# Kernel tuning notes

Measured on AMD Instinct MI355X. Metric: run time of the kernel, lower is better.

## Reference

```python
import jax, jax.numpy as jnp
import numpy as np

DIM = 1536; NH = 12; HD = DIM // NH; C = HD // 2  # C = 64
F, H, W = 12, 16, 16; S = F * H * W  # 3072 tokens
NFPB = 3       # num_frame_per_block (block-causal granularity)
LOCAL = 6      # local_attn_size in frames
SINK = 1       # sink_size in frames
EPS = 1e-06


def setup_inputs():
    key = jax.random.key(0)
    ks = jax.random.split(key, 6)
    sc = 1.0 / np.sqrt(DIM)
    x = jax.random.normal(ks[0], (1, S, DIM), jnp.float32)
    Wq = jax.random.normal(ks[1], (DIM, DIM), jnp.float32) * sc
    Wk = jax.random.normal(ks[2], (DIM, DIM), jnp.float32) * sc
    Wv = jax.random.normal(ks[3], (DIM, DIM), jnp.float32) * sc
    Wo = jax.random.normal(ks[4], (DIM, DIM), jnp.float32) * sc
    zeros = jnp.zeros((DIM,), jnp.float32); ones = jnp.ones((DIM,), jnp.float32)
    # RoPE table: unit-modulus complex freqs stored as cos/sin, shape [1024, C]
    ang = jax.random.uniform(ks[5], (1024, C), jnp.float32) * (2.0 * np.pi)
    return dict(x=x, Wq=Wq, bq=zeros, Wk=Wk, bk=zeros, Wv=Wv, bv=zeros,
                Wo=Wo, bo=zeros, gq=ones, gk=ones,
                freqs_cos=jnp.cos(ang), freqs_sin=jnp.sin(ang), f=F, h=H, w=W)


def _rms_norm(x, g):
    y = x * jax.lax.rsqrt(jnp.mean(x * x, axis=-1, keepdims=True) + EPS)
    return y * g


def _pos_table(tab, f, h, w):
    # split [1024, C] into frame/height/width parts and broadcast to [f*h*w, C]
    cf = C - 2 * (C // 3); ch = C // 3
    tf = jnp.broadcast_to(tab[:f, :cf][:, None, None, :], (f, h, w, cf))
    th = jnp.broadcast_to(tab[:h, cf:cf + ch][None, :, None, :], (f, h, w, ch))
    tw = jnp.broadcast_to(tab[:w, cf + ch:][None, None, :, :], (f, h, w, ch))
    return jnp.concatenate([tf, th, tw], axis=-1).reshape(f * h * w, C)


def _rope(x, cosp, sinp):
    # complex multiply on consecutive (real, imag) pairs along head_dim
    b, s, n, d = x.shape
    xp = x.reshape(b, s, n, d // 2, 2)
    xr, xi = xp[..., 0], xp[..., 1]
    cp = cosp[None, :, None, :]; sp = sinp[None, :, None, :]
    out = jnp.stack([xr * cp - xi * sp, xr * sp + xi * cp], axis=-1)
    return out.reshape(b, s, n, d)


def reference(x, Wq, bq, Wk, bk, Wv, bv, Wo, bo, gq, gk, freqs_cos, freqs_sin, f, h, w):
    b, s, _ = x.shape
    q = _rms_norm(x @ Wq.T + bq, gq).reshape(b, s, NH, HD)
    k = _rms_norm(x @ Wk.T + bk, gk).reshape(b, s, NH, HD)
    v = (x @ Wv.T + bv).reshape(b, s, NH, HD)
    cosp = _pos_table(freqs_cos, f, h, w)
    sinp = _pos_table(freqs_sin, f, h, w)
    rq = _rope(q, cosp, sinp)
    rk = _rope(k, cosp, sinp)
    # block mask: block-causal (bidirectional inside a frame-block) + local window + sink
    idx = jnp.arange(s)
    frame = idx // (h * w)
    blk = frame // NFPB
    qb, kb = blk[:, None], blk[None, :]
    mask = (kb <= qb) & ((((qb - kb) * NFPB) < LOCAL) | (frame[None, :] < SINK))
    scores = jnp.einsum('bqnd,bknd->bnqk', rq, rk) * (HD ** -0.5)
    scores = jnp.where(mask[None, None], scores, jnp.finfo(scores.dtype).min)
    probs = jax.nn.softmax(scores, axis=-1)
    out = jnp.einsum('bnqk,bknd->bqnd', probs, v).reshape(b, s, DIM)
    return out @ Wo.T + bo
```

## Files before the change

kernel.cpp:

```cpp
#include <hip/hip_runtime.h>
#include <stdint.h>

typedef unsigned short u16;
typedef __attribute__((ext_vector_type(8))) short bf16x8;
typedef __attribute__((ext_vector_type(4))) short bf16x4;
typedef __attribute__((ext_vector_type(4))) float f32x4;

constexpr int DMODEL = 1536;
constexpr int SEQ    = 3072;
constexpr int NHEAD  = 12;
constexpr int HDIM   = 128;

__device__ __forceinline__ u16 f2bf(float f){
  union { float f; unsigned u; } v; v.f = f;
  return (u16)((v.u + 0x7fffu + ((v.u >> 16) & 1u)) >> 16);
}

__global__ __launch_bounds__(256) void cvt4_kernel(const float* __restrict__ src,
                                                   u16* __restrict__ dst, int n4){
  int i = blockIdx.x * 256 + threadIdx.x;
  if (i < n4){
    float4 f = ((const float4*)src)[i];
    ushort4 o;
    o.x = f2bf(f.x); o.y = f2bf(f.y); o.z = f2bf(f.z); o.w = f2bf(f.w);
    ((ushort4*)dst)[i] = o;
  }
}

__device__ __forceinline__ void gload16(const u16* g, u16* l){
  __builtin_amdgcn_global_load_lds((const __attribute__((address_space(1))) void*)g,
                                   (__attribute__((address_space(3))) void*)l, 16, 0, 0);
}

__device__ __forceinline__ void gemm_core(const u16* __restrict__ A, const u16* __restrict__ W,
    const float* __restrict__ bias, float* __restrict__ C, int m0, int n0,
    u16* As, u16* Bs)
{
  const int tid  = threadIdx.x;
  const int lane = tid & 63;
  const int wv   = tid >> 6;
  const int wm   = wv & 1, wn = wv >> 1;
  const int l15  = lane & 15, lg = lane >> 4;

  f32x4 acc[4][4];
#pragma unroll
  for (int i = 0; i < 4; i++)
#pragma unroll
    for (int j = 0; j < 4; j++){ f32x4 z = {0.f,0.f,0.f,0.f}; acc[i][j] = z; }

  const int r0 = wv * 16 + (lane >> 2);
  const int r1 = (wv + 4) * 16 + (lane >> 2);
  const int cc = (lane & 3) * 8;
  const u16* Ab = A + (size_t)m0 * DMODEL;
  const u16* Wb = W + (size_t)n0 * DMODEL;

  for (int k0 = 0; k0 < DMODEL; k0 += 32){
    gload16(Ab + (size_t)r0 * DMODEL + k0 + cc, As + wv * 512);
    gload16(Ab + (size_t)r1 * DMODEL + k0 + cc, As + (wv + 4) * 512);
    gload16(Wb + (size_t)r0 * DMODEL + k0 + cc, Bs + wv * 512);
    gload16(Wb + (size_t)r1 * DMODEL + k0 + cc, Bs + (wv + 4) * 512);
    __syncthreads();

    bf16x8 af[4], bfr[4];
#pragma unroll
    for (int mi = 0; mi < 4; mi++)
      af[mi]  = *(const bf16x8*)(As + (wm * 64 + mi * 16 + l15) * 32 + lg * 8);
#pragma unroll
    for (int ni = 0; ni < 4; ni++)
      bfr[ni] = *(const bf16x8*)(Bs + (wn * 64 + ni * 16 + l15) * 32 + lg * 8);
#pragma unroll
    for (int mi = 0; mi < 4; mi++)
#pragma unroll
      for (int ni = 0; ni < 4; ni++)
        acc[mi][ni] = __builtin_amdgcn_mfma_f32_16x16x32_bf16(af[mi], bfr[ni], acc[mi][ni], 0, 0, 0);
    __syncthreads();
  }

#pragma unroll
  for (int mi = 0; mi < 4; mi++){
    int row = m0 + wm * 64 + mi * 16 + (lg << 2);
#pragma unroll
    for (int ni = 0; ni < 4; ni++){
      int col = n0 + wn * 64 + ni * 16 + l15;
      float bvv = bias[col];
#pragma unroll
      for (int r = 0; r < 4; r++)
        C[(size_t)(row + r) * DMODEL + col] = acc[mi][ni][r] + bvv;
    }
  }
}

__global__ __launch_bounds__(256) void gemm_qkv(const u16* __restrict__ xb,
    const u16* __restrict__ wqb, const u16* __restrict__ wkb, const u16* __restrict__ wvb,
    const float* __restrict__ bq, const float* __restrict__ bk, const float* __restrict__ bv,
    float* __restrict__ qf, float* __restrict__ kf, float* __restrict__ vf)
{
  __shared__ u16 As[128 * 32], Bs[128 * 32];
  int mt = blockIdx.x, nt = blockIdx.y;
  int sel = nt / 12, ntl = nt % 12;
  const u16* W = sel == 0 ? wqb : (sel == 1 ? wkb : wvb);
  const float* bias = sel == 0 ? bq : (sel == 1 ? bk : bv);
  float* C = sel == 0 ? qf : (sel == 1 ? kf : vf);
  gemm_core(xb, W, bias, C, mt * 128, ntl * 128, As, Bs);
}

__global__ __launch_bounds__(256) void gemm_o(const u16* __restrict__ ab,
    const u16* __restrict__ wob, const float* __restrict__ bo, float* __restrict__ out)
{
  __shared__ u16 As[128 * 32], Bs[128 * 32];
  gemm_core(ab, wob, bo, out, blockIdx.x * 128, blockIdx.y * 128, As, Bs);
}

__global__ __launch_bounds__(256) void rmsrope_kernel(
    const float* __restrict__ qin, const float* __restrict__ kin,
    const float* __restrict__ gq, const float* __restrict__ gk,
    const float* __restrict__ fcos, const float* __restrict__ fsin,
    u16* __restrict__ rq, u16* __restrict__ rk)
{
  int s = blockIdx.x, t = threadIdx.x;
  int fi = s >> 8, hi2 = (s >> 4) & 15, wi = s & 15;
  __shared__ float red[4];

  for (int pass = 0; pass < 2; pass++){
    const float* in = pass ? kin : qin;
    const float* g  = pass ? gk  : gq;
    u16* outp       = pass ? rk  : rq;
    const float* row = in + (size_t)s * DMODEL;

    float v[6];
    float2 a = *(const float2*)(row + t * 6);
    float2 b = *(const float2*)(row + t * 6 + 2);
    float2 c = *(const float2*)(row + t * 6 + 4);
    v[0] = a.x; v[1] = a.y; v[2] = b.x; v[3] = b.y; v[4] = c.x; v[5] = c.y;

    float ss = 0.f;
#pragma unroll
    for (int j = 0; j < 6; j++) ss += v[j] * v[j];
#pragma unroll
    for (int m = 1; m < 64; m <<= 1) ss += __shfl_xor(ss, m);
    if ((t & 63) == 0) red[t >> 6] = ss;
    __syncthreads();
    float tot = red[0] + red[1] + red[2] + red[3];
    float scale = rsqrtf(tot * (1.0f / (float)DMODEL) + 1e-6f);

#pragma unroll
    for (int p = 0; p < 3; p++){
      int i  = t * 3 + p;
      int pi = i & 63;
      int idx = pi < 22 ? fi : (pi < 43 ? hi2 : wi);
      float cv = fcos[idx * 64 + pi];
      float sv = fsin[idx * 64 + pi];
      int d = t * 6 + 2 * p;
      float xr = v[2 * p]     * scale * g[d];
      float xi = v[2 * p + 1] * scale * g[d + 1];
      outp[(size_t)s * DMODEL + d]     = f2bf(xr * cv - xi * sv);
      outp[(size_t)s * DMODEL + d + 1] = f2bf(xr * sv + xi * cv);
    }
    __syncthreads();
  }
}

__global__ __launch_bounds__(256) void transpose_v(const float* __restrict__ vf, u16* __restrict__ vt)
{
  __shared__ float tile[32][33];
  int tx = threadIdx.x & 31, ty = threadIdx.x >> 5;
  int d0 = blockIdx.x * 32;
  int s0 = blockIdx.y * 32;
#pragma unroll
  for (int j = 0; j < 4; j++)
    tile[ty + j * 8][tx] = vf[(size_t)(s0 + ty + j * 8) * DMODEL + d0 + tx];
  __syncthreads();
  int px = ((tx & 15) >> 2) * 8 + ((tx >> 4) & 1) * 4 + (tx & 3);
#pragma unroll
  for (int j = 0; j < 4; j++)
    vt[(size_t)(d0 + ty + j * 8) * SEQ + s0 + px] = f2bf(tile[tx][ty + j * 8]);
}

__global__ __launch_bounds__(256, 2) void attn_kernel(const u16* __restrict__ rq,
    const u16* __restrict__ rk, const u16* __restrict__ vt, u16* __restrict__ ao)
{
  __shared__ u16 Ks[2][8192];
  __shared__ u16 Vs[2][8192];

  const int tid  = threadIdx.x;
  const int lane = tid & 63;
  const int wv   = tid >> 6;
  const int head = blockIdx.y;
  const int grp  = blockIdx.x / 12;
  const int rem  = blockIdx.x - grp * 12;
  const int qb   = 3 - grp;
  const int q_i  = qb * 12 + rem;
  const int q0   = q_i * 64 + wv * 16;
  const int l15  = lane & 15, lg = lane >> 4;
  const int swz  = (l15 & 7) << 4;
  const float sc = 0.08838834764831845f;

  int r0s = 0, r0e = 0, r1s = 0, r1e = 0;
  if      (qb == 0){ r0e = 768; }
  else if (qb == 1){ r0e = 1536; }
  else if (qb == 2){ r0e = 256; r1s = 768;  r1e = 2304; }
  else             { r0e = 256; r1s = 1536; r1e = 3072; }
  const int nt0 = (r0e - r0s) >> 6;
  const int nt  = nt0 + ((r1e - r1s) >> 6);

  const char* rkB = (const char*)rk;
  const char* vtB = (const char*)vt;

  auto k0_of = [&](int t){ return t < nt0 ? (r0s + t * 64) : (r1s + (t - nt0) * 64); };

  auto stage = [&](int buf, int k0){
    char* Kd = (char*)Ks[buf];
    char* Vd = (char*)Vs[buf];
#pragma unroll
    for (int c = 0; c < 4; c++){
      int o = c * 4096 + wv * 1024 + lane * 16;
      int row = o >> 8, colb = o & 255;
      gload16((const u16*)(rkB + (size_t)(k0 + row) * (DMODEL * 2) + head * (HDIM * 2)
                               + (colb ^ ((row & 7) << 4))),
              (u16*)(Kd + c * 4096 + wv * 1024));
    }
#pragma unroll
    for (int c = 0; c < 4; c++){
      int o = c * 4096 + wv * 1024 + lane * 16;
      int row = o >> 7, colb = o & 127;
      gload16((const u16*)(vtB + (size_t)(head * HDIM + row) * (SEQ * 2) + (size_t)k0 * 2
                               + (colb ^ ((row & 7) << 4))),
              (u16*)(Vd + c * 4096 + wv * 1024));
    }
  };

  bf16x8 qfr[4];
  const u16* qbase = rq + (size_t)(q0 + l15) * DMODEL + head * HDIM + lg * 8;
#pragma unroll
  for (int c = 0; c < 4; c++) qfr[c] = *(const bf16x8*)(qbase + c * 32);

  f32x4 oacc[8];
#pragma unroll
  for (int i = 0; i < 8; i++){ f32x4 z = {0.f,0.f,0.f,0.f}; oacc[i] = z; }
  float l_run = 0.f;

  stage(0, k0_of(0));
  __syncthreads();

  for (int t = 0; t < nt; t++){
    int buf = t & 1;
    if (t + 1 < nt) stage(buf ^ 1, k0_of(t + 1));

    const char* Kb = (const char*)Ks[buf];
    const char* Vb = (const char*)Vs[buf];
#pragma unroll
    for (int half = 0; half < 2; half++){
      const int kt = half * 32;
      const char* kr0 = Kb + (kt + l15) * 256;
      const char* kr1 = kr0 + 16 * 256;
      bf16x8 kf0[4], kf1[4];
#pragma unroll
      for (int c = 0; c < 4; c++){
        kf0[c] = *(const bf16x8*)(kr0 + ((lg * 16 + c * 64) ^ swz));
        kf1[c] = *(const bf16x8*)(kr1 + ((lg * 16 + c * 64) ^ swz));
      }
      f32x4 s0 = {0.f,0.f,0.f,0.f}, s1 = {0.f,0.f,0.f,0.f};
      __builtin_amdgcn_s_setprio(1);
#pragma unroll
      for (int c = 0; c < 4; c++){
        s0 = __builtin_amdgcn_mfma_f32_16x16x32_bf16(kf0[c], qfr[c], s0, 0, 0, 0);
        s1 = __builtin_amdgcn_mfma_f32_16x16x32_bf16(kf1[c], qfr[c], s1, 0, 0, 0);
      }
      __builtin_amdgcn_s_setprio(0);

      bf16x8 pf;
      float lsum = 0.f;
#pragma unroll
      for (int r = 0; r < 4; r++){
        float e0 = __expf(fmaf(s0[r], sc, -12.f));
        float e1 = __expf(fmaf(s1[r], sc, -12.f));
        lsum += e0 + e1;
        pf[r]     = (short)f2bf(e0);
        pf[r + 4] = (short)f2bf(e1);
      }
      l_run += lsum;

      __builtin_amdgcn_s_setprio(1);
#pragma unroll
      for (int ch = 0; ch < 8; ch++){
        bf16x8 vf8 = *(const bf16x8*)(Vb + (ch * 16 + l15) * 128 + ((half * 64 + lg * 16) ^ swz));
        oacc[ch] = __builtin_amdgcn_mfma_f32_16x16x32_bf16(pf, vf8, oacc[ch], 0, 0, 0);
      }
      __builtin_amdgcn_s_setprio(0);
    }
    __syncthreads();
  }

  l_run += __shfl_xor(l_run, 16);
  l_run += __shfl_xor(l_run, 32);
  float li[4];
#pragma unroll
  for (int r = 0; r < 4; r++) li[r] = 1.f / __shfl(l_run, lg * 4 + r);
#pragma unroll
  for (int ch = 0; ch < 8; ch++)
#pragma unroll
    for (int r = 0; r < 4; r++)
      ao[(size_t)(q0 + lg * 4 + r) * DMODEL + head * HDIM + ch * 16 + l15] =
          f2bf(oacc[ch][r] * li[r]);
}

extern "C" void kernel_launch(void* const* d_in, const int* in_sizes, int n_in,
                              void* d_out, int out_size, void* d_ws, size_t ws_size,
                              hipStream_t stream)
{
  const float* x    = (const float*)d_in[0];
  const float* Wq   = (const float*)d_in[1];
  const float* bq   = (const float*)d_in[2];
  const float* Wk   = (const float*)d_in[3];
  const float* bk   = (const float*)d_in[4];
  const float* Wv   = (const float*)d_in[5];
  const float* bv   = (const float*)d_in[6];
  const float* Wo   = (const float*)d_in[7];
  const float* bo   = (const float*)d_in[8];
  const float* gq   = (const float*)d_in[9];
  const float* gk   = (const float*)d_in[10];
  const float* fcos = (const float*)d_in[11];
  const float* fsin = (const float*)d_in[12];
  float* out = (float*)d_out;

  char* ws = (char*)d_ws;
  size_t off = 0;
  auto alloc = [&](size_t bytes){
    void* p = ws + off;
    off += (bytes + 255) & ~(size_t)255;
    return p;
  };
  const size_t SD = (size_t)SEQ * DMODEL;
  const size_t WW = (size_t)DMODEL * DMODEL;
  u16*   xb  = (u16*)  alloc(SD * 2);
  u16*   wqb = (u16*)  alloc(WW * 2);
  u16*   wkb = (u16*)  alloc(WW * 2);
  u16*   wvb = (u16*)  alloc(WW * 2);
  u16*   wob = (u16*)  alloc(WW * 2);
  float* qf  = (float*)alloc(SD * 4);
  float* kf  = (float*)alloc(SD * 4);
  float* vf  = (float*)alloc(SD * 4);
  u16*   rq  = (u16*)  alloc(SD * 2);
  u16*   rk  = (u16*)  alloc(SD * 2);
  u16*   vt  = (u16*)  alloc(SD * 2);
  u16*   ao  = (u16*)  alloc(SD * 2);

  int nx4 = (int)(SD / 4), nw4 = (int)(WW / 4);
  cvt4_kernel<<<(nx4 + 255) / 256, 256, 0, stream>>>(x,  xb,  nx4);
  cvt4_kernel<<<(nw4 + 255) / 256, 256, 0, stream>>>(Wq, wqb, nw4);
  cvt4_kernel<<<(nw4 + 255) / 256, 256, 0, stream>>>(Wk, wkb, nw4);
  cvt4_kernel<<<(nw4 + 255) / 256, 256, 0, stream>>>(Wv, wvb, nw4);
  cvt4_kernel<<<(nw4 + 255) / 256, 256, 0, stream>>>(Wo, wob, nw4);

  gemm_qkv<<<dim3(SEQ / 128, 36), 256, 0, stream>>>(xb, wqb, wkb, wvb, bq, bk, bv, qf, kf, vf);
  rmsrope_kernel<<<SEQ, 256, 0, stream>>>(qf, kf, gq, gk, fcos, fsin, rq, rk);
  transpose_v<<<dim3(DMODEL / 32, SEQ / 32), 256, 0, stream>>>(vf, vt);
  attn_kernel<<<dim3(SEQ / 64, NHEAD), 256, 0, stream>>>(rq, rk, vt, ao);
  gemm_o<<<dim3(SEQ / 128, DMODEL / 128), 256, 0, stream>>>(ao, wob, bo, out);
}
```

Measured before the change: 339.3 us.

## Fuse conversions, double-buffer GEMM, fuse V transpose, split attention KV range

The five fp32-to-bf16 conversion launches become a single kernel. The GEMM gets a double-buffered LDS pipeline, and the V projection writes a transposed bf16 output straight from its epilogue, which removes both the fp32 V buffer and the separate transpose kernel. RMSNorm+RoPE now handles one row per wavefront with vectorised loads and stores and no block-level sync. Attention splits the key range of the heavier query blocks across two workgroups to balance load, writing partial outputs and row sums into the reused q buffer. A new reduce kernel then combines the partials and normalises them, at the cost of extra fp32 traffic and one more launch.

```diff
diff --git a/kernel.cpp b/kernel.cpp
--- a/kernel.cpp
+++ b/kernel.cpp
@@ -16,15 +16,25 @@
   return (u16)((v.u + 0x7fffu + ((v.u >> 16) & 1u)) >> 16);
 }
 
-__global__ __launch_bounds__(256) void cvt4_kernel(const float* __restrict__ src,
-                                                   u16* __restrict__ dst, int n4){
+__global__ __launch_bounds__(256) void cvt_all(
+    const float* __restrict__ x,  const float* __restrict__ wq,
+    const float* __restrict__ wk, const float* __restrict__ wv, const float* __restrict__ wo,
+    u16* __restrict__ xb, u16* __restrict__ wqb, u16* __restrict__ wkb,
+    u16* __restrict__ wvb, u16* __restrict__ wob)
+{
+  const int NX = (SEQ * DMODEL) / 4;
+  const int NW = (DMODEL * DMODEL) / 4;
   int i = blockIdx.x * 256 + threadIdx.x;
-  if (i < n4){
-    float4 f = ((const float4*)src)[i];
-    ushort4 o;
-    o.x = f2bf(f.x); o.y = f2bf(f.y); o.z = f2bf(f.z); o.w = f2bf(f.w);
-    ((ushort4*)dst)[i] = o;
-  }
+  const float* src; u16* dst; int off;
+  if      (i < NX)          { src = x;  dst = xb;  off = i; }
+  else if (i < NX + NW)     { src = wq; dst = wqb; off = i - NX; }
+  else if (i < NX + 2 * NW) { src = wk; dst = wkb; off = i - NX - NW; }
+  else if (i < NX + 3 * NW) { src = wv; dst = wvb; off = i - NX - 2 * NW; }
+  else                      { src = wo; dst = wob; off = i - NX - 3 * NW; }
+  float4 f = ((const float4*)src)[off];
+  ushort4 o;
+  o.x = f2bf(f.x); o.y = f2bf(f.y); o.z = f2bf(f.z); o.w = f2bf(f.w);
+  ((ushort4*)dst)[off] = o;
 }
 
 __device__ __forceinline__ void gload16(const u16* g, u16* l){
@@ -33,8 +43,8 @@
 }
 
 __device__ __forceinline__ void gemm_core(const u16* __restrict__ A, const u16* __restrict__ W,
-    const float* __restrict__ bias, float* __restrict__ C, int m0, int n0,
-    u16* As, u16* Bs)
+    const float* __restrict__ bias, float* __restrict__ C, u16* __restrict__ VT,
+    int m0, int n0, bool vfuse, u16* As, u16* Bs)
 {
   const int tid  = threadIdx.x;
   const int lane = tid & 63;
@@ -54,20 +64,29 @@
   const u16* Ab = A + (size_t)m0 * DMODEL;
   const u16* Wb = W + (size_t)n0 * DMODEL;
 
+  auto stageg = [&](int b, int k0){
+    gload16(Ab + (size_t)r0 * DMODEL + k0 + cc, As + b * 4096 + wv * 512);
+    gload16(Ab + (size_t)r1 * DMODEL + k0 + cc, As + b * 4096 + (wv + 4) * 512);
+    gload16(Wb + (size_t)r0 * DMODEL + k0 + cc, Bs + b * 4096 + wv * 512);
+    gload16(Wb + (size_t)r1 * DMODEL + k0 + cc, Bs + b * 4096 + (wv + 4) * 512);
+  };
+
+  stageg(0, 0);
+  __syncthreads();
+
   for (int k0 = 0; k0 < DMODEL; k0 += 32){
-    gload16(Ab + (size_t)r0 * DMODEL + k0 + cc, As + wv * 512);
-    gload16(Ab + (size_t)r1 * DMODEL + k0 + cc, As + (wv + 4) * 512);
-    gload16(Wb + (size_t)r0 * DMODEL + k0 + cc, Bs + wv * 512);
-    gload16(Wb + (size_t)r1 * DMODEL + k0 + cc, Bs + (wv + 4) * 512);
-    __syncthreads();
-
+    int b = (k0 >> 5) & 1;
+    if (k0 + 32 < DMODEL) stageg(b ^ 1, k0 + 32);
+
+    const u16* Ar = As + b * 4096;
+    const u16* Br = Bs + b * 4096;
     bf16x8 af[4], bfr[4];
 #pragma unroll
     for (int mi = 0; mi < 4; mi++)
-      af[mi]  = *(const bf16x8*)(As + (wm * 64 + mi * 16 + l15) * 32 + lg * 8);
+      af[mi]  = *(const bf16x8*)(Ar + (wm * 64 + mi * 16 + l15) * 32 + lg * 8);
 #pragma unroll
     for (int ni = 0; ni < 4; ni++)
-      bfr[ni] = *(const bf16x8*)(Bs + (wn * 64 + ni * 16 + l15) * 32 + lg * 8);
+      bfr[ni] = *(const bf16x8*)(Br + (wn * 64 + ni * 16 + l15) * 32 + lg * 8);
 #pragma unroll
     for (int mi = 0; mi < 4; mi++)
 #pragma unroll
@@ -76,16 +95,34 @@
     __syncthreads();
   }
 
-#pragma unroll
-  for (int mi = 0; mi < 4; mi++){
-    int row = m0 + wm * 64 + mi * 16 + (lg << 2);
-#pragma unroll
-    for (int ni = 0; ni < 4; ni++){
-      int col = n0 + wn * 64 + ni * 16 + l15;
-      float bvv = bias[col];
-#pragma unroll
-      for (int r = 0; r < 4; r++)
-        C[(size_t)(row + r) * DMODEL + col] = acc[mi][ni][r] + bvv;
+  if (!vfuse){
+#pragma unroll
+    for (int mi = 0; mi < 4; mi++){
+      int row = m0 + wm * 64 + mi * 16 + (lg << 2);
+#pragma unroll
+      for (int ni = 0; ni < 4; ni++){
+        int col = n0 + wn * 64 + ni * 16 + l15;
+        float bvv = bias[col];
+#pragma unroll
+        for (int r = 0; r < 4; r++)
+          C[(size_t)(row + r) * DMODEL + col] = acc[mi][ni][r] + bvv;
+      }
+    }
+  } else {
+#pragma unroll
+    for (int mi = 0; mi < 4; mi++){
+      int gbase = m0 + wm * 64 + (mi >> 1) * 32 + lg * 8 + (mi & 1) * 4;
+#pragma unroll
+      for (int ni = 0; ni < 4; ni++){
+        int d = n0 + wn * 64 + ni * 16 + l15;
+        float bvv = bias[d];
+        ushort4 o;
+        o.x = f2bf(acc[mi][ni][0] + bvv);
+        o.y = f2bf(acc[mi][ni][1] + bvv);
+        o.z = f2bf(acc[mi][ni][2] + bvv);
+        o.w = f2bf(acc[mi][ni][3] + bvv);
+        *(ushort4*)(VT + (size_t)d * SEQ + gbase) = o;
+      }
     }
   }
 }
@@ -93,22 +130,22 @@
 __global__ __launch_bounds__(256) void gemm_qkv(const u16* __restrict__ xb,
     const u16* __restrict__ wqb, const u16* __restrict__ wkb, const u16* __restrict__ wvb,
     const float* __restrict__ bq, const float* __restrict__ bk, const float* __restrict__ bv,
-    float* __restrict__ qf, float* __restrict__ kf, float* __restrict__ vf)
-{
-  __shared__ u16 As[128 * 32], Bs[128 * 32];
+    float* __restrict__ qf, float* __restrict__ kf, u16* __restrict__ vt)
+{
+  __shared__ u16 As[2 * 4096], Bs[2 * 4096];
   int mt = blockIdx.x, nt = blockIdx.y;
   int sel = nt / 12, ntl = nt % 12;
   const u16* W = sel == 0 ? wqb : (sel == 1 ? wkb : wvb);
   const float* bias = sel == 0 ? bq : (sel == 1 ? bk : bv);
-  float* C = sel == 0 ? qf : (sel == 1 ? kf : vf);
-  gemm_core(xb, W, bias, C, mt * 128, ntl * 128, As, Bs);
+  float* C = sel == 0 ? qf : kf;
+  gemm_core(xb, W, bias, C, vt, mt * 128, ntl * 128, sel == 2, As, Bs);
 }
 
 __global__ __launch_bounds__(256) void gemm_o(const u16* __restrict__ ab,
     const u16* __restrict__ wob, const float* __restrict__ bo, float* __restrict__ out)
 {
-  __shared__ u16 As[128 * 32], Bs[128 * 32];
-  gemm_core(ab, wob, bo, out, blockIdx.x * 128, blockIdx.y * 128, As, Bs);
+  __shared__ u16 As[2 * 4096], Bs[2 * 4096];
+  gemm_core(ab, wob, bo, out, nullptr, blockIdx.x * 128, blockIdx.y * 128, false, As, Bs);
 }
 
 __global__ __launch_bounds__(256) void rmsrope_kernel(
@@ -117,67 +154,53 @@
     const float* __restrict__ fcos, const float* __restrict__ fsin,
     u16* __restrict__ rq, u16* __restrict__ rk)
 {
-  int s = blockIdx.x, t = threadIdx.x;
+  int gw   = (blockIdx.x * 256 + threadIdx.x) >> 6;
+  int lane = threadIdx.x & 63;
+  int s    = gw >> 1;
+  int pass = gw & 1;
+  const float* in = pass ? kin : qin;
+  const float* g  = pass ? gk  : gq;
+  u16* outp       = pass ? rk  : rq;
+
+  const float* row = in + (size_t)s * DMODEL + lane * 24;
+  float v[24];
+#pragma unroll
+  for (int j = 0; j < 6; j++) *(float4*)(v + 4 * j) = ((const float4*)row)[j];
+
+  float ss = 0.f;
+#pragma unroll
+  for (int j = 0; j < 24; j++) ss += v[j] * v[j];
+#pragma unroll
+  for (int m = 1; m < 64; m <<= 1) ss += __shfl_xor(ss, m);
+  float scale = rsqrtf(ss * (1.0f / (float)DMODEL) + 1e-6f);
+
+  float gv[24];
+  const float* gp = g + lane * 24;
+#pragma unroll
+  for (int j = 0; j < 6; j++) *(float4*)(gv + 4 * j) = ((const float4*)gp)[j];
+
   int fi = s >> 8, hi2 = (s >> 4) & 15, wi = s & 15;
-  __shared__ float red[4];
-
-  for (int pass = 0; pass < 2; pass++){
-    const float* in = pass ? kin : qin;
-    const float* g  = pass ? gk  : gq;
-    u16* outp       = pass ? rk  : rq;
-    const float* row = in + (size_t)s * DMODEL;
-
-    float v[6];
-    float2 a = *(const float2*)(row + t * 6);
-    float2 b = *(const float2*)(row + t * 6 + 2);
-    float2 c = *(const float2*)(row + t * 6 + 4);
-    v[0] = a.x; v[1] = a.y; v[2] = b.x; v[3] = b.y; v[4] = c.x; v[5] = c.y;
-
-    float ss = 0.f;
-#pragma unroll
-    for (int j = 0; j < 6; j++) ss += v[j] * v[j];
-#pragma unroll
-    for (int m = 1; m < 64; m <<= 1) ss += __shfl_xor(ss, m);
-    if ((t & 63) == 0) red[t >> 6] = ss;
-    __syncthreads();
-    float tot = red[0] + red[1] + red[2] + red[3];
-    float scale = rsqrtf(tot * (1.0f / (float)DMODEL) + 1e-6f);
-
-#pragma unroll
-    for (int p = 0; p < 3; p++){
-      int i  = t * 3 + p;
-      int pi = i & 63;
-      int idx = pi < 22 ? fi : (pi < 43 ? hi2 : wi);
-      float cv = fcos[idx * 64 + pi];
-      float sv = fsin[idx * 64 + pi];
-      int d = t * 6 + 2 * p;
-      float xr = v[2 * p]     * scale * g[d];
-      float xi = v[2 * p + 1] * scale * g[d + 1];
-      outp[(size_t)s * DMODEL + d]     = f2bf(xr * cv - xi * sv);
-      outp[(size_t)s * DMODEL + d + 1] = f2bf(xr * sv + xi * cv);
-    }
-    __syncthreads();
+  u16 o[24];
+#pragma unroll
+  for (int jp = 0; jp < 12; jp++){
+    int i  = lane * 12 + jp;
+    int pi = i & 63;
+    int idx = pi < 22 ? fi : (pi < 43 ? hi2 : wi);
+    float cv = fcos[idx * 64 + pi];
+    float sv = fsin[idx * 64 + pi];
+    float xr = v[2 * jp]     * scale * gv[2 * jp];
+    float xi = v[2 * jp + 1] * scale * gv[2 * jp + 1];
+    o[2 * jp]     = f2bf(xr * cv - xi * sv);
+    o[2 * jp + 1] = f2bf(xr * sv + xi * cv);
   }
-}
-
-__global__ __launch_bounds__(256) void transpose_v(const float* __restrict__ vf, u16* __restrict__ vt)
-{
-  __shared__ float tile[32][33];
-  int tx = threadIdx.x & 31, ty = threadIdx.x >> 5;
-  int d0 = blockIdx.x * 32;
-  int s0 = blockIdx.y * 32;
-#pragma unroll
-  for (int j = 0; j < 4; j++)
-    tile[ty + j * 8][tx] = vf[(size_t)(s0 + ty + j * 8) * DMODEL + d0 + tx];
-  __syncthreads();
-  int px = ((tx & 15) >> 2) * 8 + ((tx >> 4) & 1) * 4 + (tx & 3);
-#pragma unroll
-  for (int j = 0; j < 4; j++)
-    vt[(size_t)(d0 + ty + j * 8) * SEQ + s0 + px] = f2bf(tile[tx][ty + j * 8]);
+  u16* op = outp + (size_t)s * DMODEL + lane * 24;
+#pragma unroll
+  for (int j = 0; j < 3; j++) *(bf16x8*)(op + 8 * j) = *(bf16x8*)(o + 8 * j);
 }
 
 __global__ __launch_bounds__(256, 2) void attn_kernel(const u16* __restrict__ rq,
-    const u16* __restrict__ rk, const u16* __restrict__ vt, u16* __restrict__ ao)
+    const u16* __restrict__ rk, const u16* __restrict__ vt,
+    float* __restrict__ pO, float* __restrict__ pl)
 {
   __shared__ u16 Ks[2][8192];
   __shared__ u16 Vs[2][8192];
@@ -186,27 +209,31 @@
   const int lane = tid & 63;
   const int wv   = tid >> 6;
   const int head = blockIdx.y;
-  const int grp  = blockIdx.x / 12;
-  const int rem  = blockIdx.x - grp * 12;
-  const int qb   = 3 - grp;
-  const int q_i  = qb * 12 + rem;
-  const int q0   = q_i * 64 + wv * 16;
+  const int bid  = blockIdx.x;
+  int qb, blk, sub;
+  if      (bid < 24){ qb = 3; blk = bid >> 1;        sub = bid & 1; }
+  else if (bid < 48){ qb = 2; blk = (bid - 24) >> 1; sub = bid & 1; }
+  else if (bid < 72){ qb = 1; blk = (bid - 48) >> 1; sub = bid & 1; }
+  else              { qb = 0; blk = bid - 72;        sub = 0; }
+  const int qblk = qb * 12 + blk;
+  const int q0   = qblk * 64 + wv * 16;
   const int l15  = lane & 15, lg = lane >> 4;
   const int swz  = (l15 & 7) << 4;
   const float sc = 0.08838834764831845f;
 
-  int r0s = 0, r0e = 0, r1s = 0, r1e = 0;
+  int r1s = 0, r1e = 0, r0e = 0;
   if      (qb == 0){ r0e = 768; }
   else if (qb == 1){ r0e = 1536; }
   else if (qb == 2){ r0e = 256; r1s = 768;  r1e = 2304; }
   else             { r0e = 256; r1s = 1536; r1e = 3072; }
-  const int nt0 = (r0e - r0s) >> 6;
+  const int nt0 = r0e >> 6;
   const int nt  = nt0 + ((r1e - r1s) >> 6);
+  const int hl  = (qb == 0) ? nt : (nt >> 1);
+  const int ts  = sub * hl, te = ts + hl;
 
   const char* rkB = (const char*)rk;
   const char* vtB = (const char*)vt;
-
-  auto k0_of = [&](int t){ return t < nt0 ? (r0s + t * 64) : (r1s + (t - nt0) * 64); };
+  auto k0_of = [&](int t){ return t < nt0 ? t * 64 : (r1s + (t - nt0) * 64); };
 
   auto stage = [&](int buf, int k0){
     char* Kd = (char*)Ks[buf];
@@ -239,12 +266,12 @@
   for (int i = 0; i < 8; i++){ f32x4 z = {0.f,0.f,0.f,0.f}; oacc[i] = z; }
   float l_run = 0.f;
 
-  stage(0, k0_of(0));
+  stage(0, k0_of(ts));
   __syncthreads();
 
-  for (int t = 0; t < nt; t++){
-    int buf = t & 1;
-    if (t + 1 < nt) stage(buf ^ 1, k0_of(t + 1));
+  for (int t = ts; t < te; t++){
+    int buf = (t - ts) & 1;
+    if (t + 1 < te) stage(buf ^ 1, k0_of(t + 1));
 
     const char* Kb = (const char*)Ks[buf];
     const char* Vb = (const char*)Vs[buf];
@@ -291,17 +318,59 @@
     __syncthreads();
   }
 
+  const size_t punit = (size_t)(head * 84 + bid);
   l_run += __shfl_xor(l_run, 16);
   l_run += __shfl_xor(l_run, 32);
-  float li[4];
-#pragma unroll
-  for (int r = 0; r < 4; r++) li[r] = 1.f / __shfl(l_run, lg * 4 + r);
+  if (lg == 0) pl[punit * 64 + wv * 16 + l15] = l_run;
+
+  float* po = pO + punit * 8192;
 #pragma unroll
   for (int ch = 0; ch < 8; ch++)
 #pragma unroll
     for (int r = 0; r < 4; r++)
-      ao[(size_t)(q0 + lg * 4 + r) * DMODEL + head * HDIM + ch * 16 + l15] =
-          f2bf(oacc[ch][r] * li[r]);
+      po[(wv * 16 + lg * 4 + r) * 128 + ch * 16 + l15] = oacc[ch][r];
+}
+
+__global__ __launch_bounds__(256) void attn_reduce(const float* __restrict__ pO,
+    const float* __restrict__ pl, u16* __restrict__ ao)
+{
+  const int qblk = blockIdx.x;
+  const int head = blockIdx.y;
+  const int qb = qblk / 12, blk = qblk % 12;
+  int b0, nu;
+  if      (qb == 0){ b0 = 72 + blk;     nu = 1; }
+  else if (qb == 1){ b0 = 48 + 2 * blk; nu = 2; }
+  else if (qb == 2){ b0 = 24 + 2 * blk; nu = 2; }
+  else             { b0 = 2 * blk;      nu = 2; }
+  const size_t u0 = (size_t)(head * 84 + b0);
+  const float* O0 = pO + u0 * 8192;
+  const float* L0 = pl + u0 * 64;
+
+  __shared__ float ls[64];
+  int t = threadIdx.x;
+  if (t < 64) ls[t] = L0[t] + (nu == 2 ? L0[64 + t] : 0.f);
+  __syncthreads();
+
+  int q = t >> 2, dc = (t & 3) * 32;
+  float inv = 1.f / ls[q];
+  const float* a0 = O0 + q * 128 + dc;
+  const float* a1 = a0 + 8192;
+  u16 buf[32];
+#pragma unroll
+  for (int j = 0; j < 32; j += 4){
+    float4 xv = *(const float4*)(a0 + j);
+    if (nu == 2){
+      float4 y = *(const float4*)(a1 + j);
+      xv.x += y.x; xv.y += y.y; xv.z += y.z; xv.w += y.w;
+    }
+    buf[j]     = f2bf(xv.x * inv);
+    buf[j + 1] = f2bf(xv.y * inv);
+    buf[j + 2] = f2bf(xv.z * inv);
+    buf[j + 3] = f2bf(xv.w * inv);
+  }
+  u16* op = ao + (size_t)(qblk * 64 + q) * DMODEL + head * HDIM + dc;
+#pragma unroll
+  for (int j = 0; j < 32; j += 8) *(bf16x8*)(op + j) = *(bf16x8*)(buf + j);
 }
 
 extern "C" void kernel_launch(void* const* d_in, const int* in_sizes, int n_in,
@@ -339,22 +408,18 @@
   u16*   wob = (u16*)  alloc(WW * 2);
   float* qf  = (float*)alloc(SD * 4);
   float* kf  = (float*)alloc(SD * 4);
-  float* vf  = (float*)alloc(SD * 4);
   u16*   rq  = (u16*)  alloc(SD * 2);
   u16*   rk  = (u16*)  alloc(SD * 2);
   u16*   vt  = (u16*)  alloc(SD * 2);
   u16*   ao  = (u16*)  alloc(SD * 2);
-
-  int nx4 = (int)(SD / 4), nw4 = (int)(WW / 4);
-  cvt4_kernel<<<(nx4 + 255) / 256, 256, 0, stream>>>(x,  xb,  nx4);
-  cvt4_kernel<<<(nw4 + 255) / 256, 256, 0, stream>>>(Wq, wqb, nw4);
-  cvt4_kernel<<<(nw4 + 255) / 256, 256, 0, stream>>>(Wk, wkb, nw4);
-  cvt4_kernel<<<(nw4 + 255) / 256, 256, 0, stream>>>(Wv, wvb, nw4);
-  cvt4_kernel<<<(nw4 + 255) / 256, 256, 0, stream>>>(Wo, wob, nw4);
-
-  gemm_qkv<<<dim3(SEQ / 128, 36), 256, 0, stream>>>(xb, wqb, wkb, wvb, bq, bk, bv, qf, kf, vf);
-  rmsrope_kernel<<<SEQ, 256, 0, stream>>>(qf, kf, gq, gk, fcos, fsin, rq, rk);
-  transpose_v<<<dim3(DMODEL / 32, SEQ / 32), 256, 0, stream>>>(vf, vt);
-  attn_kernel<<<dim3(SEQ / 64, NHEAD), 256, 0, stream>>>(rq, rk, vt, ao);
+  float* pl  = (float*)alloc((size_t)1008 * 64 * 4);
+  float* pO  = qf;
+
+  const int NX = (SEQ * DMODEL) / 4, NW = (DMODEL * DMODEL) / 4;
+  cvt_all<<<(NX + 4 * NW) / 256, 256, 0, stream>>>(x, Wq, Wk, Wv, Wo, xb, wqb, wkb, wvb, wob);
+  gemm_qkv<<<dim3(SEQ / 128, 36), 256, 0, stream>>>(xb, wqb, wkb, wvb, bq, bk, bv, qf, kf, vt);
+  rmsrope_kernel<<<(SEQ * 2) / 4, 256, 0, stream>>>(qf, kf, gq, gk, fcos, fsin, rq, rk);
+  attn_kernel<<<dim3(84, NHEAD), 256, 0, stream>>>(rq, rk, vt, pO, pl);
+  attn_reduce<<<dim3(48, NHEAD), 256, 0, stream>>>(pO, pl, ao);
   gemm_o<<<dim3(SEQ / 128, DMODEL / 128), 256, 0, stream>>>(ao, wob, bo, out);
 }
```

Result: faster. 321.7 us (-5.2%).
